# Kernel optimization log

Measured on AMD Instinct MI355X. Metric: run time of the kernel, lower is better.

## Reference

```python
import jax, jax.numpy as jnp
import numpy as np
import math

FEATURE_DIM = 128
INPUT_DIM = 2
OUTPUT_DIM = 3
SIGMA_Q = 128.0
SIGMA_LS = [16.0, 64.0, 256.0]
N_PATCHES = 256
HIDDEN = 512
HEADS = 2
DIM_HEAD = 64
ALPHA = 10.0
N_FREQ = FEATURE_DIM // (2 * INPUT_DIM)  # 32
B, HW = 8, 16384


def _omegas(sigma):
    # torch.logspace(1, log10(sigma), n): 10^1 .. sigma, n points
    return jnp.logspace(1.0, math.log10(sigma), N_FREQ, dtype=jnp.float32)


def calc_gamma(coords, omegas):
    # coords: [L, D] -> [L, D*2*n]
    arg = jnp.pi * coords[:, :, None] * omegas[None, None, :]  # [L, D, n]
    g = jnp.concatenate([jnp.sin(arg), jnp.cos(arg)], axis=-1)  # [L, D, 2n]
    return g.reshape(coords.shape[0], -1)


def setup_inputs() -> dict:
    key = jax.random.key(0)
    ks = jax.random.split(key, 16)
    w = lambda k, shape: (jax.random.normal(k, shape, dtype=jnp.float32) * 0.05)
    return {
        "x": jax.random.uniform(ks[0], (B, HW, INPUT_DIM), dtype=jnp.float32),
        "tokens": jax.random.normal(ks[1], (B, N_PATCHES, HIDDEN), dtype=jnp.float32),
        "q_W": w(ks[2], (FEATURE_DIM, HIDDEN)),
        "q_b": w(ks[3], (HIDDEN,)),
        "Wq": w(ks[4], (HIDDEN, HEADS * DIM_HEAD)),
        "Wkv": w(ks[5], (HIDDEN, 2 * HEADS * DIM_HEAD)),
        "Wo": w(ks[6], (HEADS * DIM_HEAD, HIDDEN)),
        "bo": w(ks[7], (HIDDEN,)),
        "bw_W": w(ks[8], (3, FEATURE_DIM, HIDDEN)),
        "bw_b": w(ks[9], (3, HIDDEN)),
        "mod_W": w(ks[10], (3, HIDDEN, HIDDEN)),
        "mod_b": w(ks[11], (3, HIDDEN)),
        "hv_W": w(ks[12], (2, HIDDEN, HIDDEN)),
        "hv_b": w(ks[13], (2, HIDDEN)),
        "out_W": w(ks[14], (3, HIDDEN, OUTPUT_DIM)),
        "out_b": w(ks[15], (3, OUTPUT_DIM)),
    }


def reference(x, tokens, q_W, q_b, Wq, Wkv, Wo, bo, bw_W, bw_b, mod_W, mod_b,
              hv_W, hv_b, out_W, out_b):
    b, hw = x.shape[0], x.shape[1]
    grid = x[0]  # shared query grid [HW, 2]
    patch = int(math.sqrt(N_PATCHES))  # 16

    # relative-distance bias (ALiBi-like)
    row = (grid[:, 0] * patch).astype(jnp.int32)
    col = (grid[:, 1] * patch).astype(jnp.int32)
    idx = row * patch + col  # [HW]
    m = tokens.shape[1]
    t = idx.astype(jnp.float32) / (patch * patch)
    pos = (jnp.arange(m, dtype=jnp.float32) + 0.5) / m
    bias = -ALPHA * (t[:, None] - pos[None, :]) ** 2  # [HW, m]

    # query Fourier encode + linear
    xq = calc_gamma(grid, _omegas(SIGMA_Q))  # [HW, feature_dim]
    xq = jax.nn.relu(xq @ q_W + q_b)  # [HW, hidden]

    # shared-token cross attention (queries identical across batch)
    scale = DIM_HEAD ** -0.5
    q = (xq @ Wq).reshape(hw, HEADS, DIM_HEAD)  # [HW, H, Dh]
    kv = tokens @ Wkv  # [B, m, 2*H*Dh]
    k, v = jnp.split(kv, 2, axis=-1)
    k = k.reshape(b, m, HEADS, DIM_HEAD)
    v = v.reshape(b, m, HEADS, DIM_HEAD)
    sim = jnp.einsum('qhd,bkhd->bhqk', q, k) * scale + bias[None, None]
    attn = jax.nn.softmax(sim, axis=-1)
    out = jnp.einsum('bhqk,bkhd->bqhd', attn, v).reshape(b, hw, HEADS * DIM_HEAD)
    mod = out @ Wo + bo  # [B, HW, hidden] modulation vector

    # multi-band MLPs
    mods = []
    for i in range(len(SIGMA_LS)):
        gl = calc_gamma(grid, _omegas(SIGMA_LS[i]))  # [HW, feature_dim]
        h_l = jax.nn.relu(gl @ bw_W[i] + bw_b[i])  # [HW, hidden]
        m_l = jax.nn.relu(h_l[None] + mod @ mod_W[i] + mod_b[i])  # [B, HW, hidden]
        mods.append(m_l)

    h_v = mods[0]
    total = h_v @ out_W[0] + out_b[0]
    for i in range(len(SIGMA_LS) - 1):
        h_v = jax.nn.relu((mods[i + 1] + h_v) @ hv_W[i] + hv_b[i])
        total = total + h_v @ out_W[i + 1] + out_b[i + 1]

    return total.reshape(b, hw, -1)
```

## Files before the change

kernel.cpp:

```cpp
#include <hip/hip_runtime.h>
#include <math.h>

typedef unsigned short u16;
typedef unsigned int uint;
typedef __bf16 bf16x8 __attribute__((ext_vector_type(8)));
typedef unsigned short u16x8 __attribute__((ext_vector_type(8)));
typedef float f32x4 __attribute__((ext_vector_type(4)));

#define HWQ 16384
#define PI_F 3.14159265358979323846f

#define C_X     0
#define C_TOK   262144
#define C_QW    1310720
#define C_QB    1376256
#define C_WQ    1376768
#define C_WKV   1442304
#define C_WO    1704448
#define C_BO    1769984
#define C_BWW   1770496
#define C_BWB   1967104
#define C_MODW  1968640
#define C_MODB  2755072
#define C_HVW   2756608
#define C_HVB   3280896
#define C_OUTW  3281920
#define C_OUTB  3286528
#define C_TOTAL 3286537
#define CANON_PAD 3286544

#define QWT_OFF  0
#define WQT_OFF  65536
#define WOT_OFF  131072
#define BWT_OFF  196608
#define MODT_OFF 393216
#define HVT_OFF  1179648

struct SrcPtrs { const void* p[16]; };

__device__ __forceinline__ float bs2f(u16 u){
  unsigned v = ((unsigned)u) << 16; float f; __builtin_memcpy(&f, &v, 4); return f;
}
__device__ __forceinline__ u16 f2bs(float f){
  unsigned v; __builtin_memcpy(&v, &f, 4);
  v = (v + 0x7fffu + ((v >> 16) & 1u)) >> 16;
  return (u16)v;
}
__device__ __forceinline__ f32x4 mfma16(bf16x8 a, bf16x8 b, f32x4 c){
  return __builtin_amdgcn_mfma_f32_16x16x32_bf16(a, b, c, 0, 0, 0);
}
__device__ __forceinline__ bf16x8 ld8(const u16* p){ return *(const bf16x8*)p; }
__device__ __forceinline__ void ld2lds(const u16* g, u16* l){
  __builtin_amdgcn_global_load_lds((__attribute__((address_space(1))) const uint*)g,
                                   (__attribute__((address_space(3))) uint*)l, 16, 0, 0);
}

__global__ void k_detect(const u16* qb_raw, unsigned* flag){
  __shared__ int cnt[256];
  int t = threadIdx.x;
  u16 u = qb_raw[2*t];
  int e = (u >> 7) & 0xFF;
  cnt[t] = (e >= 126) ? 1 : 0;
  __syncthreads();
  for (int s = 128; s > 0; s >>= 1){
    if (t < s) cnt[t] += cnt[t + s];
    __syncthreads();
  }
  if (t == 0) *flag = (cnt[0] >= 16) ? 1u : 0u;
}

__global__ __launch_bounds__(256) void k_convert(SrcPtrs sp, const unsigned* flag, u16* canon){
  const int offs[17] = {C_X,C_TOK,C_QW,C_QB,C_WQ,C_WKV,C_WO,C_BO,C_BWW,C_BWB,
                        C_MODW,C_MODB,C_HVW,C_HVB,C_OUTW,C_OUTB,C_TOTAL};
  int e = blockIdx.x * 256 + threadIdx.x;
  if (e >= C_TOTAL) return;
  int seg = 0;
  for (int i = 1; i < 16; i++) if (e >= offs[i]) seg = i;
  int local = e - offs[seg];
  if (*flag) canon[e] = f2bs(((const float*)sp.p[seg])[local]);
  else       canon[e] = ((const u16*)sp.p[seg])[local];
}

__global__ __launch_bounds__(256) void k_tr(const u16* canon, u16* WT){
  __shared__ u16 tile[32][33];
  int bid = blockIdx.x, t = threadIdx.x;
  const u16* src; u16* dst; int K, N, tl;
  bool kblk = (bid >= 384);
  if (bid < 384){
    int m = bid >> 6; tl = bid & 63;
    if (m == 0){ src = canon + C_QW;  dst = WT + QWT_OFF; K = 128; N = 512; }
    else if (m == 1){ src = canon + C_WQ; dst = WT + WQT_OFF; K = 512; N = 128; }
    else if (m == 2){ src = canon + C_WO; dst = WT + WOT_OFF; K = 128; N = 512; }
    else { src = canon + C_BWW + (m-3)*65536; dst = WT + BWT_OFF + (m-3)*65536; K = 128; N = 512; }
  } else if (bid < 1152){
    int m = (bid - 384) >> 8; tl = (bid - 384) & 255;
    src = canon + C_MODW + m*262144; dst = WT + MODT_OFF + m*262144; K = 512; N = 512;
  } else {
    int m = (bid - 1152) >> 8; tl = (bid - 1152) & 255;
    src = canon + C_HVW + m*262144; dst = WT + HVT_OFF + m*262144; K = 512; N = 512;
  }
  int kt = K >> 5;
  int k0 = (tl % kt) * 32, n0 = (tl / kt) * 32;
  int tx = t & 31, ty = t >> 5;
  for (int r = 0; r < 4; r++)
    tile[ty + r*8][tx] = src[(size_t)(k0 + ty + r*8) * N + n0 + tx];
  __syncthreads();
  if (!kblk){
    for (int r = 0; r < 4; r++)
      dst[(size_t)(n0 + ty + r*8) * K + k0 + tx] = tile[tx][ty + r*8];
  } else {
    u16* d2 = dst + (size_t)(k0 >> 5)*16384;
    for (int r = 0; r < 4; r++)
      d2[(n0 + ty + r*8)*32 + tx] = tile[tx][ty + r*8];
  }
}

__global__ __launch_bounds__(256) void k_kv(const u16* canon, u16* kpart, u16* vT){
  int b = blockIdx.x >> 8, kk = blockIdx.x & 255, t = threadIdx.x;
  const u16* tok = canon + C_TOK;
  const u16* Wkv = canon + C_WKV;
  __shared__ float tk[512];
  const u16* tr = tok + ((size_t)(b*256 + kk)) * 512;
  tk[t] = bs2f(tr[t]); tk[t+256] = bs2f(tr[t+256]);
  __syncthreads();
  float acc = 0.f;
  for (int k = 0; k < 512; k++) acc += tk[k] * bs2f(Wkv[k*256 + t]);
  if (t < 128) kpart[((size_t)(b*256 + kk))*128 + t] = f2bs(acc);
  else vT[((size_t)b*128 + (t-128))*256 + kk] = f2bs(acc);
}

__global__ __launch_bounds__(256) void k_query(const u16* canon, const float* xraw,
      const unsigned* flag, const u16* WT, u16* qvecB, u16* hlB){
  int t = threadIdx.x, q0 = blockIdx.x * 16;
  const u16* q_b = canon + C_QB;
  const u16* bw_b= canon + C_BWB;
  int lane = t & 63, wv = t >> 6, l15 = lane & 15, q4 = lane >> 4;
  __shared__ __align__(16) u16 g[16*136];
  __shared__ __align__(16) u16 xql[16*520];
  __shared__ float cco[32];
  __shared__ float omg[32];
  for (int e = t; e < 16*136; e += 256) g[e] = 0;
  for (int e = t; e < 16*520; e += 256) xql[e] = 0;
  if (t < 32) cco[t] = (*flag) ? xraw[q0*2 + t] : bs2f(canon[C_X + q0*2 + t]);
  if (t < 32) omg[t] = (float)pow(10.0, 1.0 + t * ((2.1072099696478683 - 1.0)/31.0));
  __syncthreads();
  for (int i = 0; i < 8; i++){
    int id = i*256 + t, qi = id >> 7, f = id & 127;
    int d = f >> 6, r = f & 63, fi = r & 31;
    float arg = PI_F * cco[qi*2 + d] * omg[fi];
    g[qi*136 + f] = f2bs((r < 32) ? sinf(arg) : cosf(arg));
  }
  __syncthreads();
  {
    const u16* Bm = WT + QWT_OFF;
    for (int nt = 0; nt < 8; nt++){
      f32x4 acc = {0.f,0.f,0.f,0.f};
      int c = wv*128 + nt*16 + l15;
      for (int ks = 0; ks < 4; ks++){
        bf16x8 a  = ld8(g + l15*136 + ks*32 + q4*8);
        bf16x8 bb = ld8(Bm + (size_t)c*128 + ks*32 + q4*8);
        acc = mfma16(a, bb, acc);
      }
      float qb = bs2f(q_b[c]);
      for (int rg = 0; rg < 4; rg++){
        int row = q4*4 + rg;
        xql[row*520 + c] = f2bs(fmaxf(acc[rg] + qb, 0.f));
      }
    }
  }
  __syncthreads();
  {
    const u16* Bm = WT + WQT_OFF;
    for (int nh = 0; nh < 2; nh++){
      f32x4 acc = {0.f,0.f,0.f,0.f};
      int c = wv*32 + nh*16 + l15;
      for (int ks = 0; ks < 16; ks++){
        bf16x8 a  = ld8(xql + l15*520 + ks*32 + q4*8);
        bf16x8 bb = ld8(Bm + (size_t)c*512 + ks*32 + q4*8);
        acc = mfma16(a, bb, acc);
      }
      for (int rg = 0; rg < 4; rg++)
        g[(q4*4 + rg)*128 + c] = f2bs(acc[rg]);
    }
    __syncthreads();
    {
      int rr = t >> 4, cc = (t & 15)*8;
      *(u16x8*)(qvecB + (size_t)(q0 + rr)*128 + cc) = *(const u16x8*)(g + rr*128 + cc);
    }
  }
  const double LG[3] = {1.2041199826559248, 1.8061799739838869, 2.4082399653118496};
  for (int ib = 0; ib < 3; ib++){
    __syncthreads();
    if (t < 32) omg[t] = (float)pow(10.0, 1.0 + t * ((LG[ib] - 1.0)/31.0));
    __syncthreads();
    for (int i = 0; i < 8; i++){
      int id = i*256 + t, qi = id >> 7, f = id & 127;
      int d = f >> 6, r = f & 63, fi = r & 31;
      float arg = PI_F * cco[qi*2 + d] * omg[fi];
      g[qi*136 + f] = f2bs((r < 32) ? sinf(arg) : cosf(arg));
    }
    __syncthreads();
    const u16* Bm = WT + BWT_OFF + ib*65536;
    for (int nt = 0; nt < 8; nt++){
      f32x4 acc = {0.f,0.f,0.f,0.f};
      int c = wv*128 + nt*16 + l15;
      for (int ks = 0; ks < 4; ks++){
        bf16x8 a  = ld8(g + l15*136 + ks*32 + q4*8);
        bf16x8 bb = ld8(Bm + (size_t)c*128 + ks*32 + q4*8);
        acc = mfma16(a, bb, acc);
      }
      float bias = bs2f(bw_b[ib*512 + c]);
      for (int rg = 0; rg < 4; rg++)
        xql[(q4*4 + rg)*520 + c] = f2bs(fmaxf(acc[rg] + bias, 0.f));
    }
    __syncthreads();
    for (int it = 0; it < 4; it++){
      int rr = it*4 + (t >> 6), cc = (t & 63)*8;
      *(u16x8*)(hlB + ((size_t)ib*HWQ + q0 + rr)*512 + cc) = *(const u16x8*)(xql + rr*520 + cc);
    }
  }
}

__global__ __launch_bounds__(256) void k_attn(const u16* canon, const float* xraw,
      const unsigned* flag, const u16* qvecB, const u16* kpart, const u16* vT,
      const u16* WT, u16* modB){
  int t = threadIdx.x;
  int b = blockIdx.x & 7, qt = blockIdx.x >> 3, q0 = qt*32;
  const u16* bo = canon + C_BO;
  int lane = t & 63, wv = t >> 6, l15 = lane & 15, q4 = lane >> 4;
  __shared__ __align__(16) u16 ql[32*136];
  __shared__ __align__(16) u16 pl[32*264];
  __shared__ __align__(16) float pf[32*264];
  __shared__ __align__(16) u16 ot[32*136];
  __shared__ float tqs[32];
  __shared__ float red[256];
  __shared__ float rst[32];
  for (int e = t; e < 32*136; e += 256){ ql[e] = 0; ot[e] = 0; }
  for (int e = t; e < 32*264; e += 256) pl[e] = 0;
  __syncthreads();
  for (int i = 0; i < 16; i++){
    int id = i*256 + t, qi = id >> 7, c = id & 127;
    ql[qi*136 + c] = qvecB[(size_t)(q0 + qi)*128 + c];
  }
  if (t < 32){
    float c0, c1;
    if (*flag){ c0 = xraw[(q0+t)*2]; c1 = xraw[(q0+t)*2 + 1]; }
    else { c0 = bs2f(canon[C_X + (q0+t)*2]); c1 = bs2f(canon[C_X + (q0+t)*2 + 1]); }
    int rr = (int)(c0*16.f), cc = (int)(c1*16.f);
    tqs[t] = (float)(rr*16 + cc) * (1.f/256.f);
  }
  __syncthreads();
  for (int h = 0; h < 2; h++){
    f32x4 sac[2][4];
    for (int mt = 0; mt < 2; mt++) for (int nt = 0; nt < 4; nt++) sac[mt][nt] = (f32x4){0.f,0.f,0.f,0.f};
    const u16* kb = kpart + (size_t)b*256*128 + h*64;
    for (int ks = 0; ks < 2; ks++){
      bf16x8 a0 = ld8(ql + l15*136 + h*64 + ks*32 + q4*8);
      bf16x8 a1 = ld8(ql + (16+l15)*136 + h*64 + ks*32 + q4*8);
      for (int nt = 0; nt < 4; nt++){
        int kk = wv*64 + nt*16 + l15;
        bf16x8 bb = ld8(kb + (size_t)kk*128 + ks*32 + q4*8);
        sac[0][nt] = mfma16(a0, bb, sac[0][nt]);
        sac[1][nt] = mfma16(a1, bb, sac[1][nt]);
      }
    }
    for (int mt = 0; mt < 2; mt++) for (int nt = 0; nt < 4; nt++){
      int kk = wv*64 + nt*16 + l15;
      float pos = ((float)kk + 0.5f) * (1.f/256.f);
      for (int rg = 0; rg < 4; rg++){
        int row = mt*16 + q4*4 + rg;
        float dd = tqs[row] - pos;
        pf[row*264 + kk] = sac[mt][nt][rg]*0.125f - 10.f*dd*dd;
      }
    }
    __syncthreads();
    {
      int r = t >> 3, i = t & 7;
      float* pr = pf + r*264 + i*32;
      u16* po = pl + r*264 + i*32;
      float m = -1e30f;
      for (int j = 0; j < 32; j++) m = fmaxf(m, pr[j]);
      red[t] = m;
      __syncthreads();
      if (t < 32){ float mm = red[t*8];
        for (int j = 1; j < 8; j++) mm = fmaxf(mm, red[t*8+j]);
        rst[t] = mm; }
      __syncthreads();
      float mm = rst[r], sum = 0.f;
      for (int j = 0; j < 32; j++){ float e = expf(pr[j] - mm); pr[j] = e; sum += e; }
      red[t] = sum;
      __syncthreads();
      if (t < 32){ float ss = 0.f;
        for (int j = 0; j < 8; j++) ss += red[t*8+j];
        rst[t] = 1.f/ss; }
      __syncthreads();
      float inv = rst[r];
      for (int j = 0; j < 32; j++) po[j] = f2bs(pr[j] * inv);
    }
    __syncthreads();
    f32x4 oac[2] = {(f32x4){0.f,0.f,0.f,0.f}, (f32x4){0.f,0.f,0.f,0.f}};
    const u16* vb = vT + ((size_t)b*128 + h*64)*256;
    int dl = wv*16 + l15;
    for (int ks = 0; ks < 8; ks++){
      bf16x8 a0 = ld8(pl + l15*264 + ks*32 + q4*8);
      bf16x8 a1 = ld8(pl + (16+l15)*264 + ks*32 + q4*8);
      bf16x8 bb = ld8(vb + (size_t)dl*256 + ks*32 + q4*8);
      oac[0] = mfma16(a0, bb, oac[0]);
      oac[1] = mfma16(a1, bb, oac[1]);
    }
    for (int mt = 0; mt < 2; mt++) for (int rg = 0; rg < 4; rg++){
      int row = mt*16 + q4*4 + rg;
      ot[row*136 + h*64 + dl] = f2bs(oac[mt][rg]);
    }
    __syncthreads();
  }
  u16* stg = (u16*)pf;
  const u16* wob = WT + WOT_OFF;
  for (int nt = 0; nt < 8; nt++){
    f32x4 mac[2] = {(f32x4){0.f,0.f,0.f,0.f}, (f32x4){0.f,0.f,0.f,0.f}};
    int c = wv*128 + nt*16 + l15;
    for (int ks = 0; ks < 4; ks++){
      bf16x8 a0 = ld8(ot + l15*136 + ks*32 + q4*8);
      bf16x8 a1 = ld8(ot + (16+l15)*136 + ks*32 + q4*8);
      bf16x8 bb = ld8(wob + (size_t)c*128 + ks*32 + q4*8);
      mac[0] = mfma16(a0, bb, mac[0]);
      mac[1] = mfma16(a1, bb, mac[1]);
    }
    float bv = bs2f(bo[c]);
    for (int mt = 0; mt < 2; mt++) for (int rg = 0; rg < 4; rg++){
      int row = mt*16 + q4*4 + rg;
      stg[row*512 + c] = f2bs(mac[mt][rg] + bv);
    }
  }
  __syncthreads();
  for (int it = 0; it < 8; it++){
    int rr = it*4 + (t >> 6), cc = (t & 63)*8;
    int q = q0 + rr;
    size_t off = (size_t)(q >> 3)*32768 + (size_t)(cc >> 5)*2048
               + (size_t)((q & 7)*8 + b)*32 + (cc & 31);
    *(u16x8*)(modB + off) = *(const u16x8*)(stg + rr*512 + cc);
  }
}


#define ZACC for (int mt = 0; mt < 4; mt++) for (int nt = 0; nt < 4; nt++) acc[mt][nt] = (f32x4){0.f,0.f,0.f,0.f};

#define XLI(row, c) (((c) >> 5)*2048 + (row)*32 + ((c) & 31))

#define GEMMX(Abuf, Bgl)                                                         \
  { ZACC                                                                         \
    const u16* bptr = (Bgl) + (size_t)(w*64 + l15)*32 + q4*8;                    \
    const u16* aptr = (Abuf) + l15*32 + q4*8;                                    \
    _Pragma("unroll 1")                                                          \
    for (int ks = 0; ks < 16; ks++){                                             \
      bf16x8 b0 = ld8(bptr + ks*16384 +    0);                                   \
      bf16x8 b1 = ld8(bptr + ks*16384 +  512);                                   \
      bf16x8 b2 = ld8(bptr + ks*16384 + 1024);                                   \
      bf16x8 b3 = ld8(bptr + ks*16384 + 1536);                                   \
      bf16x8 a0 = ld8(aptr + ks*2048 +    0);                                    \
      bf16x8 a1 = ld8(aptr + ks*2048 +  512);                                    \
      bf16x8 a2 = ld8(aptr + ks*2048 + 1024);                                    \
      bf16x8 a3 = ld8(aptr + ks*2048 + 1536);                                    \
      acc[0][0] = mfma16(a0, b0, acc[0][0]);                                     \
      acc[0][1] = mfma16(a0, b1, acc[0][1]);                                     \
      acc[0][2] = mfma16(a0, b2, acc[0][2]);                                     \
      acc[0][3] = mfma16(a0, b3, acc[0][3]);                                     \
      acc[1][0] = mfma16(a1, b0, acc[1][0]);                                     \
      acc[1][1] = mfma16(a1, b1, acc[1][1]);                                     \
      acc[1][2] = mfma16(a1, b2, acc[1][2]);                                     \
      acc[1][3] = mfma16(a1, b3, acc[1][3]);                                     \
      acc[2][0] = mfma16(a2, b0, acc[2][0]);                                     \
      acc[2][1] = mfma16(a2, b1, acc[2][1]);                                     \
      acc[2][2] = mfma16(a2, b2, acc[2][2]);                                     \
      acc[2][3] = mfma16(a2, b3, acc[2][3]);                                     \
      acc[3][0] = mfma16(a3, b0, acc[3][0]);                                     \
      acc[3][1] = mfma16(a3, b1, acc[3][1]);                                     \
      acc[3][2] = mfma16(a3, b2, acc[3][2]);                                     \
      acc[3][3] = mfma16(a3, b3, acc[3][3]);                                     \
    } }

#define PROJ_REDUCE                                                              \
  __syncthreads();                                                               \
  if (t < 192){ float s = 0.f;                                                   \
    for (int w2 = 0; w2 < 8; w2++) s += pscr[w2*192 + t];                        \
    totrow[t] += s; }                                                            \
  __syncthreads();

__global__ __launch_bounds__(512, 2) void k_bands3(const u16* canon, const u16* modB,
      const u16* WT, const u16* hlB, const unsigned* flag, void* outv){
  int t = threadIdx.x, rgp = blockIdx.x;
  int lane = t & 63, w = t >> 6, l15 = lane & 15, q4 = lane >> 4;
  __shared__ __align__(16) u16 XL[16*64*32];
  __shared__ __align__(16) u16 AL[16*64*32];
  __shared__ float pscr[1536];
  __shared__ float totrow[192];
  if (t < 192){
    int o = t - (t/3)*3;
    totrow[t] = bs2f(canon[C_OUTB + o]) + bs2f(canon[C_OUTB + 3 + o]) + bs2f(canon[C_OUTB + 6 + o]);
  }
  {
    const u16* src = modB + (size_t)rgp*32768;
    for (int i = 0; i < 8; i++)
      ld2lds(src + i*4096 + w*512 + lane*8, AL + i*4096 + w*512);
  }
  const u16* hl0 = hlB;
  const u16* hl1 = hlB + (size_t)HWQ*512;
  const u16* hl2 = hlB + (size_t)2*HWQ*512;
  int qbase = rgp*8;
  f32x4 acc[4][4];
  __syncthreads();

  GEMMX(AL, WT + MODT_OFF);
  {
    float ow[4][3], bias[4];
    for (int nt = 0; nt < 4; nt++){
      int c = w*64 + nt*16 + l15;
      bias[nt] = bs2f(canon[C_MODB + c]);
      for (int o = 0; o < 3; o++) ow[nt][o] = bs2f(canon[C_OUTW + c*3 + o]);
    }
    for (int mt = 0; mt < 4; mt++) for (int rg = 0; rg < 4; rg++){
      int row = mt*16 + q4*4 + rg;
      int q = qbase + (row >> 3);
      float p0 = 0.f, p1 = 0.f, p2 = 0.f;
      for (int nt = 0; nt < 4; nt++){
        int c = w*64 + nt*16 + l15;
        float v = acc[mt][nt][rg] + bias[nt] + bs2f(hl0[(size_t)q*512 + c]);
        v = fmaxf(v, 0.f);
        XL[XLI(row, c)] = f2bs(v);
        p0 += v*ow[nt][0]; p1 += v*ow[nt][1]; p2 += v*ow[nt][2];
      }
      for (int m = 1; m < 16; m <<= 1){
        p0 += __shfl_xor(p0, m, 64); p1 += __shfl_xor(p1, m, 64); p2 += __shfl_xor(p2, m, 64);
      }
      if (l15 == 0){
        pscr[w*192 + row*3 + 0] = p0;
        pscr[w*192 + row*3 + 1] = p1;
        pscr[w*192 + row*3 + 2] = p2;
      }
    }
  }
  PROJ_REDUCE;

  GEMMX(AL, WT + MODT_OFF + 262144);
  {
    float bias[4];
    for (int nt = 0; nt < 4; nt++) bias[nt] = bs2f(canon[C_MODB + 512 + w*64 + nt*16 + l15]);
    for (int mt = 0; mt < 4; mt++) for (int rg = 0; rg < 4; rg++){
      int row = mt*16 + q4*4 + rg;
      int q = qbase + (row >> 3);
      for (int nt = 0; nt < 4; nt++){
        int c = w*64 + nt*16 + l15;
        float v = acc[mt][nt][rg] + bias[nt] + bs2f(hl1[(size_t)q*512 + c]);
        v = fmaxf(v, 0.f) + bs2f(XL[XLI(row, c)]);
        XL[XLI(row, c)] = f2bs(v);
      }
    }
  }
  __syncthreads();

  GEMMX(XL, WT + HVT_OFF);
  __syncthreads();
  {
    float ow[4][3], bias[4];
    for (int nt = 0; nt < 4; nt++){
      int c = w*64 + nt*16 + l15;
      bias[nt] = bs2f(canon[C_HVB + c]);
      for (int o = 0; o < 3; o++) ow[nt][o] = bs2f(canon[C_OUTW + 1536 + c*3 + o]);
    }
    for (int mt = 0; mt < 4; mt++) for (int rg = 0; rg < 4; rg++){
      int row = mt*16 + q4*4 + rg;
      float p0 = 0.f, p1 = 0.f, p2 = 0.f;
      for (int nt = 0; nt < 4; nt++){
        int c = w*64 + nt*16 + l15;
        float v = fmaxf(acc[mt][nt][rg] + bias[nt], 0.f);
        XL[XLI(row, c)] = f2bs(v);
        p0 += v*ow[nt][0]; p1 += v*ow[nt][1]; p2 += v*ow[nt][2];
      }
      for (int m = 1; m < 16; m <<= 1){
        p0 += __shfl_xor(p0, m, 64); p1 += __shfl_xor(p1, m, 64); p2 += __shfl_xor(p2, m, 64);
      }
      if (l15 == 0){
        pscr[w*192 + row*3 + 0] = p0;
        pscr[w*192 + row*3 + 1] = p1;
        pscr[w*192 + row*3 + 2] = p2;
      }
    }
  }
  PROJ_REDUCE;

  GEMMX(AL, WT + MODT_OFF + 524288);
  {
    float bias[4];
    for (int nt = 0; nt < 4; nt++) bias[nt] = bs2f(canon[C_MODB + 1024 + w*64 + nt*16 + l15]);
    for (int mt = 0; mt < 4; mt++) for (int rg = 0; rg < 4; rg++){
      int row = mt*16 + q4*4 + rg;
      int q = qbase + (row >> 3);
      for (int nt = 0; nt < 4; nt++){
        int c = w*64 + nt*16 + l15;
        float v = acc[mt][nt][rg] + bias[nt] + bs2f(hl2[(size_t)q*512 + c]);
        v = fmaxf(v, 0.f) + bs2f(XL[XLI(row, c)]);
        XL[XLI(row, c)] = f2bs(v);
      }
    }
  }
  __syncthreads();

  GEMMX(XL, WT + HVT_OFF + 262144);
  {
    float ow[4][3], bias[4];
    for (int nt = 0; nt < 4; nt++){
      int c = w*64 + nt*16 + l15;
      bias[nt] = bs2f(canon[C_HVB + 512 + c]);
      for (int o = 0; o < 3; o++) ow[nt][o] = bs2f(canon[C_OUTW + 3072 + c*3 + o]);
    }
    for (int mt = 0; mt < 4; mt++) for (int rg = 0; rg < 4; rg++){
      int row = mt*16 + q4*4 + rg;
      float p0 = 0.f, p1 = 0.f, p2 = 0.f;
      for (int nt = 0; nt < 4; nt++){
        float v = fmaxf(acc[mt][nt][rg] + bias[nt], 0.f);
        p0 += v*ow[nt][0]; p1 += v*ow[nt][1]; p2 += v*ow[nt][2];
      }
      for (int m = 1; m < 16; m <<= 1){
        p0 += __shfl_xor(p0, m, 64); p1 += __shfl_xor(p1, m, 64); p2 += __shfl_xor(p2, m, 64);
      }
      if (l15 == 0){
        pscr[w*192 + row*3 + 0] = p0;
        pscr[w*192 + row*3 + 1] = p1;
        pscr[w*192 + row*3 + 2] = p2;
      }
    }
  }
  PROJ_REDUCE;

  if (t < 192){
    int row = t / 3, o = t - (t/3)*3;
    int gr = rgp*64 + row;
    int b = gr & 7, q = gr >> 3;
    size_t idx = ((size_t)b*HWQ + q)*3 + o;
    if (*flag) ((float*)outv)[idx] = totrow[t];
    else       ((u16*)outv)[idx]   = f2bs(totrow[t]);
  }
}

extern "C" void kernel_launch(void* const* d_in, const int* in_sizes, int n_in,
                              void* d_out, int out_size, void* d_ws, size_t ws_size,
                              hipStream_t stream){
  (void)in_sizes; (void)n_in; (void)out_size;

  u16* wsp   = (u16*)d_ws;
  unsigned* flag = (unsigned*)wsp;
  u16* canon = wsp + 8;
  u16* WT    = canon + CANON_PAD;
  u16* kpart = WT + 1703936;
  u16* vT    = kpart + 262144;
  u16* qvecB = vT + 262144;
  u16* hlB   = qvecB + 2097152;
  u16* modB  = hlB + 25165824;
  if (ws_size < 199773250ULL) return;

  SrcPtrs sp;
  for (int i = 0; i < 16; i++) sp.p[i] = d_in[i];
  const float* xraw = (const float*)d_in[0];

  k_detect <<<1, 256, 0, stream>>>((const u16*)d_in[3], flag);
  k_convert<<<(C_TOTAL + 255)/256, 256, 0, stream>>>(sp, flag, canon);
  k_tr     <<<1664, 256, 0, stream>>>(canon, WT);
  k_kv     <<<2048, 256, 0, stream>>>(canon, kpart, vT);
  k_query  <<<1024, 256, 0, stream>>>(canon, xraw, flag, WT, qvecB, hlB);
  k_attn   <<<4096, 256, 0, stream>>>(canon, xraw, flag, qvecB, kpart, vT, WT, modB);
  k_bands3 <<<2048, 512, 0, stream>>>(canon, modB, WT, hlB, flag, d_out);
}
```

Baseline: 919.8 us.

## Pair independent band GEMMs into dual-accumulator passes and swizzle LDS A layout

The five sequential 64x512x512 GEMMs in the band kernel become three passes. mod GEMMs 0 and 1 share one A-tile pass, and the hv0 GEMM is paired with mod GEMM 2. Both paired GEMMs accumulate into two register tile sets, which removes intermediate LDS round-trips and some barriers. The LDS and modB layout is also re-tiled so each lane's 8-element A fragment comes from a 16-row by 8-column sub-block, intended to cut LDS bank conflicts. Doubling the accumulators (32 f32x4) raises register pressure under launch_bounds(512,2), which risks spills or lower occupancy.

```diff
diff --git a/kernel.cpp b/kernel.cpp
--- a/kernel.cpp
+++ b/kernel.cpp
@@ -336,47 +336,78 @@
   for (int it = 0; it < 8; it++){
     int rr = it*4 + (t >> 6), cc = (t & 63)*8;
     int q = q0 + rr;
-    size_t off = (size_t)(q >> 3)*32768 + (size_t)(cc >> 5)*2048
-               + (size_t)((q & 7)*8 + b)*32 + (cc & 31);
+    int rgp = q >> 3, r = (q & 7)*8 + b;
+    size_t off = (size_t)rgp*32768 + (size_t)(cc >> 5)*2048 + (size_t)(r >> 4)*512
+               + (size_t)((cc >> 3) & 3)*128 + (size_t)(r & 15)*8;
     *(u16x8*)(modB + off) = *(const u16x8*)(stg + rr*512 + cc);
   }
 }
 
 
-#define ZACC for (int mt = 0; mt < 4; mt++) for (int nt = 0; nt < 4; nt++) acc[mt][nt] = (f32x4){0.f,0.f,0.f,0.f};
-
-#define XLI(row, c) (((c) >> 5)*2048 + (row)*32 + ((c) & 31))
-
-#define GEMMX(Abuf, Bgl)                                                         \
-  { ZACC                                                                         \
-    const u16* bptr = (Bgl) + (size_t)(w*64 + l15)*32 + q4*8;                    \
-    const u16* aptr = (Abuf) + l15*32 + q4*8;                                    \
+#define ZACC2 for (int mt = 0; mt < 4; mt++) for (int nt = 0; nt < 4; nt++){ \
+  accA[mt][nt] = (f32x4){0.f,0.f,0.f,0.f}; accB[mt][nt] = (f32x4){0.f,0.f,0.f,0.f}; }
+
+#define XLI(row, c) (((c) >> 5)*2048 + (((row) >> 4))*512 + ((((c) >> 3) & 3))*128 + (((row) & 15))*8 + ((c) & 7))
+
+#define MM16(ACC, A0,A1,A2,A3, B0,B1,B2,B3)                                      \
+  ACC[0][0]=mfma16(A0,B0,ACC[0][0]); ACC[0][1]=mfma16(A0,B1,ACC[0][1]);          \
+  ACC[0][2]=mfma16(A0,B2,ACC[0][2]); ACC[0][3]=mfma16(A0,B3,ACC[0][3]);          \
+  ACC[1][0]=mfma16(A1,B0,ACC[1][0]); ACC[1][1]=mfma16(A1,B1,ACC[1][1]);          \
+  ACC[1][2]=mfma16(A1,B2,ACC[1][2]); ACC[1][3]=mfma16(A1,B3,ACC[1][3]);          \
+  ACC[2][0]=mfma16(A2,B0,ACC[2][0]); ACC[2][1]=mfma16(A2,B1,ACC[2][1]);          \
+  ACC[2][2]=mfma16(A2,B2,ACC[2][2]); ACC[2][3]=mfma16(A2,B3,ACC[2][3]);          \
+  ACC[3][0]=mfma16(A3,B0,ACC[3][0]); ACC[3][1]=mfma16(A3,B1,ACC[3][1]);          \
+  ACC[3][2]=mfma16(A3,B2,ACC[3][2]); ACC[3][3]=mfma16(A3,B3,ACC[3][3]);
+
+#define GEMM2A(Abuf, Bg0, Bg1)                                                   \
+  { ZACC2                                                                        \
+    const u16* b0p = (Bg0) + (size_t)(w*64 + l15)*32 + q4*8;                     \
+    const u16* b1p = (Bg1) + (size_t)(w*64 + l15)*32 + q4*8;                     \
+    const u16* ap  = (Abuf) + q4*128 + l15*8;                                    \
     _Pragma("unroll 1")                                                          \
     for (int ks = 0; ks < 16; ks++){                                             \
-      bf16x8 b0 = ld8(bptr + ks*16384 +    0);                                   \
-      bf16x8 b1 = ld8(bptr + ks*16384 +  512);                                   \
-      bf16x8 b2 = ld8(bptr + ks*16384 + 1024);                                   \
-      bf16x8 b3 = ld8(bptr + ks*16384 + 1536);                                   \
-      bf16x8 a0 = ld8(aptr + ks*2048 +    0);                                    \
-      bf16x8 a1 = ld8(aptr + ks*2048 +  512);                                    \
-      bf16x8 a2 = ld8(aptr + ks*2048 + 1024);                                    \
-      bf16x8 a3 = ld8(aptr + ks*2048 + 1536);                                    \
-      acc[0][0] = mfma16(a0, b0, acc[0][0]);                                     \
-      acc[0][1] = mfma16(a0, b1, acc[0][1]);                                     \
-      acc[0][2] = mfma16(a0, b2, acc[0][2]);                                     \
-      acc[0][3] = mfma16(a0, b3, acc[0][3]);                                     \
-      acc[1][0] = mfma16(a1, b0, acc[1][0]);                                     \
-      acc[1][1] = mfma16(a1, b1, acc[1][1]);                                     \
-      acc[1][2] = mfma16(a1, b2, acc[1][2]);                                     \
-      acc[1][3] = mfma16(a1, b3, acc[1][3]);                                     \
-      acc[2][0] = mfma16(a2, b0, acc[2][0]);                                     \
-      acc[2][1] = mfma16(a2, b1, acc[2][1]);                                     \
-      acc[2][2] = mfma16(a2, b2, acc[2][2]);                                     \
-      acc[2][3] = mfma16(a2, b3, acc[2][3]);                                     \
-      acc[3][0] = mfma16(a3, b0, acc[3][0]);                                     \
-      acc[3][1] = mfma16(a3, b1, acc[3][1]);                                     \
-      acc[3][2] = mfma16(a3, b2, acc[3][2]);                                     \
-      acc[3][3] = mfma16(a3, b3, acc[3][3]);                                     \
+      bf16x8 u0=ld8(b0p+ks*16384), u1=ld8(b0p+ks*16384+512),                     \
+             u2=ld8(b0p+ks*16384+1024), u3=ld8(b0p+ks*16384+1536);               \
+      bf16x8 v0=ld8(b1p+ks*16384), v1=ld8(b1p+ks*16384+512),                     \
+             v2=ld8(b1p+ks*16384+1024), v3=ld8(b1p+ks*16384+1536);               \
+      bf16x8 a0=ld8(ap+ks*2048), a1=ld8(ap+ks*2048+512),                         \
+             a2=ld8(ap+ks*2048+1024), a3=ld8(ap+ks*2048+1536);                   \
+      MM16(accA, a0,a1,a2,a3, u0,u1,u2,u3)                                       \
+      MM16(accB, a0,a1,a2,a3, v0,v1,v2,v3)                                       \
+    } }
+
+#define GEMM2B(Ab0, Bg0, Ab1, Bg1)                                               \
+  { ZACC2                                                                        \
+    const u16* b0p = (Bg0) + (size_t)(w*64 + l15)*32 + q4*8;                     \
+    const u16* b1p = (Bg1) + (size_t)(w*64 + l15)*32 + q4*8;                     \
+    const u16* a0p = (Ab0) + q4*128 + l15*8;                                     \
+    const u16* a1p = (Ab1) + q4*128 + l15*8;                                     \
+    _Pragma("unroll 1")                                                          \
+    for (int ks = 0; ks < 16; ks++){                                             \
+      bf16x8 u0=ld8(b0p+ks*16384), u1=ld8(b0p+ks*16384+512),                     \
+             u2=ld8(b0p+ks*16384+1024), u3=ld8(b0p+ks*16384+1536);               \
+      bf16x8 v0=ld8(b1p+ks*16384), v1=ld8(b1p+ks*16384+512),                     \
+             v2=ld8(b1p+ks*16384+1024), v3=ld8(b1p+ks*16384+1536);               \
+      bf16x8 x0=ld8(a0p+ks*2048), x1=ld8(a0p+ks*2048+512),                       \
+             x2=ld8(a0p+ks*2048+1024), x3=ld8(a0p+ks*2048+1536);                 \
+      bf16x8 y0=ld8(a1p+ks*2048), y1=ld8(a1p+ks*2048+512),                       \
+             y2=ld8(a1p+ks*2048+1024), y3=ld8(a1p+ks*2048+1536);                 \
+      MM16(accA, x0,x1,x2,x3, u0,u1,u2,u3)                                       \
+      MM16(accB, y0,y1,y2,y3, v0,v1,v2,v3)                                       \
+    } }
+
+#define GEMMC(Abuf, Bgl)                                                         \
+  { for (int mt = 0; mt < 4; mt++) for (int nt = 0; nt < 4; nt++)                \
+      accA[mt][nt] = (f32x4){0.f,0.f,0.f,0.f};                                   \
+    const u16* bptr = (Bgl) + (size_t)(w*64 + l15)*32 + q4*8;                    \
+    const u16* ap   = (Abuf) + q4*128 + l15*8;                                   \
+    _Pragma("unroll 1")                                                          \
+    for (int ks = 0; ks < 16; ks++){                                             \
+      bf16x8 u0=ld8(bptr+ks*16384), u1=ld8(bptr+ks*16384+512),                   \
+             u2=ld8(bptr+ks*16384+1024), u3=ld8(bptr+ks*16384+1536);             \
+      bf16x8 a0=ld8(ap+ks*2048), a1=ld8(ap+ks*2048+512),                         \
+             a2=ld8(ap+ks*2048+1024), a3=ld8(ap+ks*2048+1536);                   \
+      MM16(accA, a0,a1,a2,a3, u0,u1,u2,u3)                                       \
     } }
 
 #define PROJ_REDUCE                                                              \
@@ -407,15 +438,16 @@
   const u16* hl1 = hlB + (size_t)HWQ*512;
   const u16* hl2 = hlB + (size_t)2*HWQ*512;
   int qbase = rgp*8;
-  f32x4 acc[4][4];
-  __syncthreads();
-
-  GEMMX(AL, WT + MODT_OFF);
+  f32x4 accA[4][4], accB[4][4];
+  __syncthreads();
+
+  GEMM2A(AL, WT + MODT_OFF, WT + MODT_OFF + 262144);
   {
-    float ow[4][3], bias[4];
+    float ow[4][3], b0v[4], b1v[4];
     for (int nt = 0; nt < 4; nt++){
       int c = w*64 + nt*16 + l15;
-      bias[nt] = bs2f(canon[C_MODB + c]);
+      b0v[nt] = bs2f(canon[C_MODB + c]);
+      b1v[nt] = bs2f(canon[C_MODB + 512 + c]);
       for (int o = 0; o < 3; o++) ow[nt][o] = bs2f(canon[C_OUTW + c*3 + o]);
     }
     for (int mt = 0; mt < 4; mt++) for (int rg = 0; rg < 4; rg++){
@@ -424,10 +456,12 @@
       float p0 = 0.f, p1 = 0.f, p2 = 0.f;
       for (int nt = 0; nt < 4; nt++){
         int c = w*64 + nt*16 + l15;
-        float v = acc[mt][nt][rg] + bias[nt] + bs2f(hl0[(size_t)q*512 + c]);
-        v = fmaxf(v, 0.f);
-        XL[XLI(row, c)] = f2bs(v);
-        p0 += v*ow[nt][0]; p1 += v*ow[nt][1]; p2 += v*ow[nt][2];
+        float v1 = accA[mt][nt][rg] + b0v[nt] + bs2f(hl0[(size_t)q*512 + c]);
+        v1 = fmaxf(v1, 0.f);
+        float v2 = accB[mt][nt][rg] + b1v[nt] + bs2f(hl1[(size_t)q*512 + c]);
+        v2 = fmaxf(v2, 0.f) + v1;
+        XL[XLI(row, c)] = f2bs(v2);
+        p0 += v1*ow[nt][0]; p1 += v1*ow[nt][1]; p2 += v1*ow[nt][2];
       }
       for (int m = 1; m < 16; m <<= 1){
         p0 += __shfl_xor(p0, m, 64); p1 += __shfl_xor(p1, m, 64); p2 += __shfl_xor(p2, m, 64);
@@ -441,83 +475,53 @@
   }
   PROJ_REDUCE;
 
-  GEMMX(AL, WT + MODT_OFF + 262144);
+  GEMM2B(XL, WT + HVT_OFF, AL, WT + MODT_OFF + 524288);
+  __syncthreads();
   {
-    float bias[4];
-    for (int nt = 0; nt < 4; nt++) bias[nt] = bs2f(canon[C_MODB + 512 + w*64 + nt*16 + l15]);
+    float ow[4][3], hb[4], b2v[4];
+    for (int nt = 0; nt < 4; nt++){
+      int c = w*64 + nt*16 + l15;
+      hb[nt]  = bs2f(canon[C_HVB + c]);
+      b2v[nt] = bs2f(canon[C_MODB + 1024 + c]);
+      for (int o = 0; o < 3; o++) ow[nt][o] = bs2f(canon[C_OUTW + 1536 + c*3 + o]);
+    }
     for (int mt = 0; mt < 4; mt++) for (int rg = 0; rg < 4; rg++){
       int row = mt*16 + q4*4 + rg;
       int q = qbase + (row >> 3);
+      float p0 = 0.f, p1 = 0.f, p2 = 0.f;
       for (int nt = 0; nt < 4; nt++){
         int c = w*64 + nt*16 + l15;
-        float v = acc[mt][nt][rg] + bias[nt] + bs2f(hl1[(size_t)q*512 + c]);
-        v = fmaxf(v, 0.f) + bs2f(XL[XLI(row, c)]);
-        XL[XLI(row, c)] = f2bs(v);
-      }
-    }
-  }
-  __syncthreads();
-
-  GEMMX(XL, WT + HVT_OFF);
-  __syncthreads();
+        float v3 = fmaxf(accA[mt][nt][rg] + hb[nt], 0.f);
+        float v4 = accB[mt][nt][rg] + b2v[nt] + bs2f(hl2[(size_t)q*512 + c]);
+        v4 = fmaxf(v4, 0.f) + v3;
+        XL[XLI(row, c)] = f2bs(v4);
+        p0 += v3*ow[nt][0]; p1 += v3*ow[nt][1]; p2 += v3*ow[nt][2];
+      }
+      for (int m = 1; m < 16; m <<= 1){
+        p0 += __shfl_xor(p0, m, 64); p1 += __shfl_xor(p1, m, 64); p2 += __shfl_xor(p2, m, 64);
+      }
+      if (l15 == 0){
+        pscr[w*192 + row*3 + 0] = p0;
+        pscr[w*192 + row*3 + 1] = p1;
+        pscr[w*192 + row*3 + 2] = p2;
+      }
+    }
+  }
+  PROJ_REDUCE;
+
+  GEMMC(XL, WT + HVT_OFF + 262144);
   {
-    float ow[4][3], bias[4];
+    float ow[4][3], hb[4];
     for (int nt = 0; nt < 4; nt++){
       int c = w*64 + nt*16 + l15;
-      bias[nt] = bs2f(canon[C_HVB + c]);
-      for (int o = 0; o < 3; o++) ow[nt][o] = bs2f(canon[C_OUTW + 1536 + c*3 + o]);
+      hb[nt] = bs2f(canon[C_HVB + 512 + c]);
+      for (int o = 0; o < 3; o++) ow[nt][o] = bs2f(canon[C_OUTW + 3072 + c*3 + o]);
     }
     for (int mt = 0; mt < 4; mt++) for (int rg = 0; rg < 4; rg++){
       int row = mt*16 + q4*4 + rg;
       float p0 = 0.f, p1 = 0.f, p2 = 0.f;
       for (int nt = 0; nt < 4; nt++){
-        int c = w*64 + nt*16 + l15;
-        float v = fmaxf(acc[mt][nt][rg] + bias[nt], 0.f);
-        XL[XLI(row, c)] = f2bs(v);
-        p0 += v*ow[nt][0]; p1 += v*ow[nt][1]; p2 += v*ow[nt][2];
-      }
-      for (int m = 1; m < 16; m <<= 1){
-        p0 += __shfl_xor(p0, m, 64); p1 += __shfl_xor(p1, m, 64); p2 += __shfl_xor(p2, m, 64);
-      }
-      if (l15 == 0){
-        pscr[w*192 + row*3 + 0] = p0;
-        pscr[w*192 + row*3 + 1] = p1;
-        pscr[w*192 + row*3 + 2] = p2;
-      }
-    }
-  }
-  PROJ_REDUCE;
-
-  GEMMX(AL, WT + MODT_OFF + 524288);
-  {
-    float bias[4];
-    for (int nt = 0; nt < 4; nt++) bias[nt] = bs2f(canon[C_MODB + 1024 + w*64 + nt*16 + l15]);
-    for (int mt = 0; mt < 4; mt++) for (int rg = 0; rg < 4; rg++){
-      int row = mt*16 + q4*4 + rg;
-      int q = qbase + (row >> 3);
-      for (int nt = 0; nt < 4; nt++){
-        int c = w*64 + nt*16 + l15;
-        float v = acc[mt][nt][rg] + bias[nt] + bs2f(hl2[(size_t)q*512 + c]);
-        v = fmaxf(v, 0.f) + bs2f(XL[XLI(row, c)]);
-        XL[XLI(row, c)] = f2bs(v);
-      }
-    }
-  }
-  __syncthreads();
-
-  GEMMX(XL, WT + HVT_OFF + 262144);
-  {
-    float ow[4][3], bias[4];
-    for (int nt = 0; nt < 4; nt++){
-      int c = w*64 + nt*16 + l15;
-      bias[nt] = bs2f(canon[C_HVB + 512 + c]);
-      for (int o = 0; o < 3; o++) ow[nt][o] = bs2f(canon[C_OUTW + 3072 + c*3 + o]);
-    }
-    for (int mt = 0; mt < 4; mt++) for (int rg = 0; rg < 4; rg++){
-      int row = mt*16 + q4*4 + rg;
-      float p0 = 0.f, p1 = 0.f, p2 = 0.f;
-      for (int nt = 0; nt < 4; nt++){
-        float v = fmaxf(acc[mt][nt][rg] + bias[nt], 0.f);
+        float v = fmaxf(accA[mt][nt][rg] + hb[nt], 0.f);
         p0 += v*ow[nt][0]; p1 += v*ow[nt][1]; p2 += v*ow[nt][2];
       }
       for (int m = 1; m < 16; m <<= 1){
```

Measured after the change: 910.1 us (median of 2 runs). Within noise of the previous version (-1.1%).

## Double rows per block in bands kernel and read modulation A-tiles from global

Applied to the files above, without the earlier changes.

The fused band-MLP kernel now handles 128 rows per block instead of 64, halving the grid and doubling reuse of each loaded weight B-fragment across eight M-tiles. The modulation A-operand is no longer staged into LDS; it is read directly from global memory in a new fragment-friendly layout written by the attention kernel. XL is re-laid out so each lane's 8-element fragment is contiguous. This cuts weight reloads and LDS footprint, at the cost of 128 accumulator registers per thread, which may lower occupancy or cause spills, and of uncached global A reads on every GEMM.

```diff
diff --git a/kernel.cpp b/kernel.cpp
--- a/kernel.cpp
+++ b/kernel.cpp
@@ -50,10 +50,6 @@
   return __builtin_amdgcn_mfma_f32_16x16x32_bf16(a, b, c, 0, 0, 0);
 }
 __device__ __forceinline__ bf16x8 ld8(const u16* p){ return *(const bf16x8*)p; }
-__device__ __forceinline__ void ld2lds(const u16* g, u16* l){
-  __builtin_amdgcn_global_load_lds((__attribute__((address_space(1))) const uint*)g,
-                                   (__attribute__((address_space(3))) uint*)l, 16, 0, 0);
-}
 
 __global__ void k_detect(const u16* qb_raw, unsigned* flag){
   __shared__ int cnt[256];
@@ -336,53 +332,61 @@
   for (int it = 0; it < 8; it++){
     int rr = it*4 + (t >> 6), cc = (t & 63)*8;
     int q = q0 + rr;
-    size_t off = (size_t)(q >> 3)*32768 + (size_t)(cc >> 5)*2048
-               + (size_t)((q & 7)*8 + b)*32 + (cc & 31);
+    int rgp = q >> 3, r = (q & 7)*8 + b;
+    size_t off = (size_t)rgp*32768 + (size_t)(cc >> 5)*2048 + (size_t)(r >> 4)*512
+               + (size_t)((cc >> 3) & 3)*128 + (size_t)(r & 15)*8;
     *(u16x8*)(modB + off) = *(const u16x8*)(stg + rr*512 + cc);
   }
 }
 
 
-#define ZACC for (int mt = 0; mt < 4; mt++) for (int nt = 0; nt < 4; nt++) acc[mt][nt] = (f32x4){0.f,0.f,0.f,0.f};
-
-#define XLI(row, c) (((c) >> 5)*2048 + (row)*32 + ((c) & 31))
-
-#define GEMMX(Abuf, Bgl)                                                         \
+#define XLI(row, c) (((c) >> 5)*4096 + (((row) >> 4))*512 + ((((c) >> 3) & 3))*128 + (((row) & 15))*8 + ((c) & 7))
+
+#define ZACC for (int mt = 0; mt < 8; mt++) for (int nt = 0; nt < 4; nt++) acc[mt][nt] = (f32x4){0.f,0.f,0.f,0.f};
+
+#define GEMMG(Bgl)                                                               \
   { ZACC                                                                         \
     const u16* bptr = (Bgl) + (size_t)(w*64 + l15)*32 + q4*8;                    \
-    const u16* aptr = (Abuf) + l15*32 + q4*8;                                    \
     _Pragma("unroll 1")                                                          \
     for (int ks = 0; ks < 16; ks++){                                             \
       bf16x8 b0 = ld8(bptr + ks*16384 +    0);                                   \
       bf16x8 b1 = ld8(bptr + ks*16384 +  512);                                   \
       bf16x8 b2 = ld8(bptr + ks*16384 + 1024);                                   \
       bf16x8 b3 = ld8(bptr + ks*16384 + 1536);                                   \
-      bf16x8 a0 = ld8(aptr + ks*2048 +    0);                                    \
-      bf16x8 a1 = ld8(aptr + ks*2048 +  512);                                    \
-      bf16x8 a2 = ld8(aptr + ks*2048 + 1024);                                    \
-      bf16x8 a3 = ld8(aptr + ks*2048 + 1536);                                    \
-      acc[0][0] = mfma16(a0, b0, acc[0][0]);                                     \
-      acc[0][1] = mfma16(a0, b1, acc[0][1]);                                     \
-      acc[0][2] = mfma16(a0, b2, acc[0][2]);                                     \
-      acc[0][3] = mfma16(a0, b3, acc[0][3]);                                     \
-      acc[1][0] = mfma16(a1, b0, acc[1][0]);                                     \
-      acc[1][1] = mfma16(a1, b1, acc[1][1]);                                     \
-      acc[1][2] = mfma16(a1, b2, acc[1][2]);                                     \
-      acc[1][3] = mfma16(a1, b3, acc[1][3]);                                     \
-      acc[2][0] = mfma16(a2, b0, acc[2][0]);                                     \
-      acc[2][1] = mfma16(a2, b1, acc[2][1]);                                     \
-      acc[2][2] = mfma16(a2, b2, acc[2][2]);                                     \
-      acc[2][3] = mfma16(a2, b3, acc[2][3]);                                     \
-      acc[3][0] = mfma16(a3, b0, acc[3][0]);                                     \
-      acc[3][1] = mfma16(a3, b1, acc[3][1]);                                     \
-      acc[3][2] = mfma16(a3, b2, acc[3][2]);                                     \
-      acc[3][3] = mfma16(a3, b3, acc[3][3]);                                     \
-    } }
+      for (int g = 0; g < 2; g++){                                               \
+        const u16* ap = (g ? ag1 : ag0) + ks*2048;                               \
+        for (int mtl = 0; mtl < 4; mtl++){                                       \
+          bf16x8 af = ld8(ap + mtl*512);                                         \
+          int mt = g*4 + mtl;                                                    \
+          acc[mt][0] = mfma16(af, b0, acc[mt][0]);                               \
+          acc[mt][1] = mfma16(af, b1, acc[mt][1]);                               \
+          acc[mt][2] = mfma16(af, b2, acc[mt][2]);                               \
+          acc[mt][3] = mfma16(af, b3, acc[mt][3]);                               \
+        }                                                                        \
+      } } }
+
+#define GEMML(Bgl)                                                               \
+  { ZACC                                                                         \
+    const u16* bptr = (Bgl) + (size_t)(w*64 + l15)*32 + q4*8;                    \
+    const u16* ap0  = XL + q4*128 + l15*8;                                       \
+    _Pragma("unroll 1")                                                          \
+    for (int ks = 0; ks < 16; ks++){                                             \
+      bf16x8 b0 = ld8(bptr + ks*16384 +    0);                                   \
+      bf16x8 b1 = ld8(bptr + ks*16384 +  512);                                   \
+      bf16x8 b2 = ld8(bptr + ks*16384 + 1024);                                   \
+      bf16x8 b3 = ld8(bptr + ks*16384 + 1536);                                   \
+      for (int mt = 0; mt < 8; mt++){                                            \
+        bf16x8 af = ld8(ap0 + ks*4096 + mt*512);                                 \
+        acc[mt][0] = mfma16(af, b0, acc[mt][0]);                                 \
+        acc[mt][1] = mfma16(af, b1, acc[mt][1]);                                 \
+        acc[mt][2] = mfma16(af, b2, acc[mt][2]);                                 \
+        acc[mt][3] = mfma16(af, b3, acc[mt][3]);                                 \
+      } } }
 
 #define PROJ_REDUCE                                                              \
   __syncthreads();                                                               \
-  if (t < 192){ float s = 0.f;                                                   \
-    for (int w2 = 0; w2 < 8; w2++) s += pscr[w2*192 + t];                        \
+  if (t < 384){ float s = 0.f;                                                   \
+    for (int w2 = 0; w2 < 8; w2++) s += pscr[w2*384 + t];                        \
     totrow[t] += s; }                                                            \
   __syncthreads();
 
@@ -390,27 +394,23 @@
       const u16* WT, const u16* hlB, const unsigned* flag, void* outv){
   int t = threadIdx.x, rgp = blockIdx.x;
   int lane = t & 63, w = t >> 6, l15 = lane & 15, q4 = lane >> 4;
-  __shared__ __align__(16) u16 XL[16*64*32];
-  __shared__ __align__(16) u16 AL[16*64*32];
-  __shared__ float pscr[1536];
-  __shared__ float totrow[192];
-  if (t < 192){
+  __shared__ __align__(16) u16 XL[16*128*32];
+  __shared__ float pscr[3072];
+  __shared__ float totrow[384];
+  if (t < 384){
     int o = t - (t/3)*3;
     totrow[t] = bs2f(canon[C_OUTB + o]) + bs2f(canon[C_OUTB + 3 + o]) + bs2f(canon[C_OUTB + 6 + o]);
   }
-  {
-    const u16* src = modB + (size_t)rgp*32768;
-    for (int i = 0; i < 8; i++)
-      ld2lds(src + i*4096 + w*512 + lane*8, AL + i*4096 + w*512);
-  }
+  const u16* ag0 = modB + (size_t)(rgp*2    )*32768 + q4*128 + l15*8;
+  const u16* ag1 = modB + (size_t)(rgp*2 + 1)*32768 + q4*128 + l15*8;
   const u16* hl0 = hlB;
   const u16* hl1 = hlB + (size_t)HWQ*512;
   const u16* hl2 = hlB + (size_t)2*HWQ*512;
-  int qbase = rgp*8;
-  f32x4 acc[4][4];
-  __syncthreads();
-
-  GEMMX(AL, WT + MODT_OFF);
+  int qbase = rgp*16;
+  f32x4 acc[8][4];
+  __syncthreads();
+
+  GEMMG(WT + MODT_OFF);
   {
     float ow[4][3], bias[4];
     for (int nt = 0; nt < 4; nt++){
@@ -418,7 +418,7 @@
       bias[nt] = bs2f(canon[C_MODB + c]);
       for (int o = 0; o < 3; o++) ow[nt][o] = bs2f(canon[C_OUTW + c*3 + o]);
     }
-    for (int mt = 0; mt < 4; mt++) for (int rg = 0; rg < 4; rg++){
+    for (int mt = 0; mt < 8; mt++) for (int rg = 0; rg < 4; rg++){
       int row = mt*16 + q4*4 + rg;
       int q = qbase + (row >> 3);
       float p0 = 0.f, p1 = 0.f, p2 = 0.f;
@@ -433,19 +433,19 @@
         p0 += __shfl_xor(p0, m, 64); p1 += __shfl_xor(p1, m, 64); p2 += __shfl_xor(p2, m, 64);
       }
       if (l15 == 0){
-        pscr[w*192 + row*3 + 0] = p0;
-        pscr[w*192 + row*3 + 1] = p1;
-        pscr[w*192 + row*3 + 2] = p2;
+        pscr[w*384 + row*3 + 0] = p0;
+        pscr[w*384 + row*3 + 1] = p1;
+        pscr[w*384 + row*3 + 2] = p2;
       }
     }
   }
   PROJ_REDUCE;
 
-  GEMMX(AL, WT + MODT_OFF + 262144);
+  GEMMG(WT + MODT_OFF + 262144);
   {
     float bias[4];
     for (int nt = 0; nt < 4; nt++) bias[nt] = bs2f(canon[C_MODB + 512 + w*64 + nt*16 + l15]);
-    for (int mt = 0; mt < 4; mt++) for (int rg = 0; rg < 4; rg++){
+    for (int mt = 0; mt < 8; mt++) for (int rg = 0; rg < 4; rg++){
       int row = mt*16 + q4*4 + rg;
       int q = qbase + (row >> 3);
       for (int nt = 0; nt < 4; nt++){
@@ -458,7 +458,7 @@
   }
   __syncthreads();
 
-  GEMMX(XL, WT + HVT_OFF);
+  GEMML(WT + HVT_OFF);
   __syncthreads();
   {
     float ow[4][3], bias[4];
@@ -467,7 +467,7 @@
       bias[nt] = bs2f(canon[C_HVB + c]);
       for (int o = 0; o < 3; o++) ow[nt][o] = bs2f(canon[C_OUTW + 1536 + c*3 + o]);
     }
-    for (int mt = 0; mt < 4; mt++) for (int rg = 0; rg < 4; rg++){
+    for (int mt = 0; mt < 8; mt++) for (int rg = 0; rg < 4; rg++){
       int row = mt*16 + q4*4 + rg;
       float p0 = 0.f, p1 = 0.f, p2 = 0.f;
       for (int nt = 0; nt < 4; nt++){
@@ -480,19 +480,19 @@
         p0 += __shfl_xor(p0, m, 64); p1 += __shfl_xor(p1, m, 64); p2 += __shfl_xor(p2, m, 64);
       }
       if (l15 == 0){
-        pscr[w*192 + row*3 + 0] = p0;
-        pscr[w*192 + row*3 + 1] = p1;
-        pscr[w*192 + row*3 + 2] = p2;
+        pscr[w*384 + row*3 + 0] = p0;
+        pscr[w*384 + row*3 + 1] = p1;
+        pscr[w*384 + row*3 + 2] = p2;
       }
     }
   }
   PROJ_REDUCE;
 
-  GEMMX(AL, WT + MODT_OFF + 524288);
+  GEMMG(WT + MODT_OFF + 524288);
   {
     float bias[4];
     for (int nt = 0; nt < 4; nt++) bias[nt] = bs2f(canon[C_MODB + 1024 + w*64 + nt*16 + l15]);
-    for (int mt = 0; mt < 4; mt++) for (int rg = 0; rg < 4; rg++){
+    for (int mt = 0; mt < 8; mt++) for (int rg = 0; rg < 4; rg++){
       int row = mt*16 + q4*4 + rg;
       int q = qbase + (row >> 3);
       for (int nt = 0; nt < 4; nt++){
@@ -505,7 +505,7 @@
   }
   __syncthreads();
 
-  GEMMX(XL, WT + HVT_OFF + 262144);
+  GEMML(WT + HVT_OFF + 262144);
   {
     float ow[4][3], bias[4];
     for (int nt = 0; nt < 4; nt++){
@@ -513,7 +513,7 @@
       bias[nt] = bs2f(canon[C_HVB + 512 + c]);
       for (int o = 0; o < 3; o++) ow[nt][o] = bs2f(canon[C_OUTW + 3072 + c*3 + o]);
     }
-    for (int mt = 0; mt < 4; mt++) for (int rg = 0; rg < 4; rg++){
+    for (int mt = 0; mt < 8; mt++) for (int rg = 0; rg < 4; rg++){
       int row = mt*16 + q4*4 + rg;
       float p0 = 0.f, p1 = 0.f, p2 = 0.f;
       for (int nt = 0; nt < 4; nt++){
@@ -524,17 +524,17 @@
         p0 += __shfl_xor(p0, m, 64); p1 += __shfl_xor(p1, m, 64); p2 += __shfl_xor(p2, m, 64);
       }
       if (l15 == 0){
-        pscr[w*192 + row*3 + 0] = p0;
-        pscr[w*192 + row*3 + 1] = p1;
-        pscr[w*192 + row*3 + 2] = p2;
+        pscr[w*384 + row*3 + 0] = p0;
+        pscr[w*384 + row*3 + 1] = p1;
+        pscr[w*384 + row*3 + 2] = p2;
       }
     }
   }
   PROJ_REDUCE;
 
-  if (t < 192){
+  if (t < 384){
     int row = t / 3, o = t - (t/3)*3;
-    int gr = rgp*64 + row;
+    int gr = rgp*128 + row;
     int b = gr & 7, q = gr >> 3;
     size_t idx = ((size_t)b*HWQ + q)*3 + o;
     if (*flag) ((float*)outv)[idx] = totrow[t];
@@ -568,5 +568,5 @@
   k_kv     <<<2048, 256, 0, stream>>>(canon, kpart, vT);
   k_query  <<<1024, 256, 0, stream>>>(canon, xraw, flag, WT, qvecB, hlB);
   k_attn   <<<4096, 256, 0, stream>>>(canon, xraw, flag, qvecB, kpart, vT, WT, modB);
-  k_bands3 <<<2048, 512, 0, stream>>>(canon, modB, WT, hlB, flag, d_out);
-}
+  k_bands3 <<<1024, 512, 0, stream>>>(canon, modB, WT, hlB, flag, d_out);
+}
```

New measurement: 1.398 ms. 52.0% more time.
